# Performance work log

Measured on AMD Instinct MI355X. Metric: run time of the kernel, lower is better.

The kernel has to match this reference:

```python
import jax, jax.numpy as jnp
import numpy as np

VOCAB, EBD, ATT_H, R, T, IMG_C = 50257, 512, 512, 196, 1024, 512


def setup_inputs() -> dict:
    key = jax.random.key(0)
    ks = jax.random.split(key, 10)
    question = jax.random.randint(ks[0], (T,), 0, VOCAB)
    img_feat = jax.random.normal(ks[1], (R, IMG_C), dtype=jnp.float32)
    emb_table = (jax.random.normal(ks[2], (VOCAB, EBD), dtype=jnp.float32) * 0.02).at[0].set(0.0)  # padding_idx=0
    W_img = jax.random.normal(ks[3], (EBD, IMG_C), dtype=jnp.float32) * (1.0 / np.sqrt(IMG_C))
    b_img = jnp.zeros((EBD,), dtype=jnp.float32)
    W_ai = jax.random.normal(ks[4], (ATT_H, EBD), dtype=jnp.float32) * (1.0 / np.sqrt(EBD))  # att_img, no bias
    W_aw = jax.random.normal(ks[5], (ATT_H, EBD), dtype=jnp.float32) * (1.0 / np.sqrt(EBD))  # att_word
    b_aw = jnp.zeros((ATT_H,), dtype=jnp.float32)
    w_att = jax.random.normal(ks[6], (ATT_H,), dtype=jnp.float32) * (1.0 / np.sqrt(ATT_H))  # att -> scalar
    b_att = jnp.zeros((), dtype=jnp.float32)
    return {"question": question, "img_feat": img_feat, "emb_table": emb_table,
            "W_img": W_img, "b_img": b_img, "W_ai": W_ai, "W_aw": W_aw,
            "b_aw": b_aw, "w_att": w_att, "b_att": b_att}


def reference(question, img_feat, emb_table, W_img, b_img, W_ai, W_aw, b_aw, w_att, b_att):
    # img_feature = relu(Linear(512 -> ebd)(vgg_regions));  [R, EBD]
    img = jax.nn.relu(img_feat @ W_img.T + b_img)
    # per-word embeddings  [T, EBD]
    E = emb_table[question]
    # additive attention: tanh(attImg[r] + attWord[t]) . w_att + b_att  -> [T, R]
    AI = img @ W_ai.T                       # [R, H]
    AW = E @ W_aw.T + b_aw                  # [T, H]
    scores = jnp.einsum('trh,h->tr', jnp.tanh(AI[None, :, :] + AW[:, None, :]), w_att) + b_att
    w = jax.nn.softmax(scores, axis=-1)     # softmax over regions, [T, R]
    # weighted sum of img features, divided by n_regions (faithful to original)
    ctx = (w @ img) / img.shape[0]          # [T, EBD]
    # attedInput: concat(new_img_feature, word_emd)  [T, 2*EBD]
    return jnp.concatenate([ctx, E], axis=-1)
```

## Files before the change

### kernel.cpp

```cpp
#include <hip/hip_runtime.h>

#define PRESCALE 2.8853900817779268f

typedef short s16;
typedef unsigned short u16;
typedef unsigned int u32;
typedef __attribute__((ext_vector_type(8))) short short8v;
typedef __attribute__((ext_vector_type(4))) float f4;

#if __has_builtin(__builtin_amdgcn_exp2f)
#define EXP2(x) __builtin_amdgcn_exp2f(x)
#else
static __device__ inline float exp2_raw(float x){ float r; asm("v_exp_f32 %0, %1":"=v"(r):"v"(x)); return r; }
#define EXP2(x) exp2_raw(x)
#endif
#if __has_builtin(__builtin_amdgcn_rcpf)
#define RCP(x) __builtin_amdgcn_rcpf(x)
#else
static __device__ inline float rcp_raw(float x){ float r; asm("v_rcp_f32 %0, %1":"=v"(r):"v"(x)); return r; }
#define RCP(x) rcp_raw(x)
#endif

__device__ inline u32 cvt2(float lo, float hi){
  u32 r; asm("v_cvt_pk_bf16_f32 %0, %1, %2" : "=v"(r) : "v"(lo), "v"(hi)); return r;
}
__device__ inline f4 ldf4(const float* p){ return *reinterpret_cast<const f4*>(p); }
__device__ inline short8v cvt8(f4 a, f4 b){
  union { u32 u[4]; short8v s; } x;
  x.u[0] = cvt2(a.x, a.y); x.u[1] = cvt2(a.z, a.w);
  x.u[2] = cvt2(b.x, b.y); x.u[3] = cvt2(b.z, b.w);
  return x.s;
}

__global__ __launch_bounds__(256) void k_front2(
    const int* __restrict__ question, const float* __restrict__ img_feat,
    const float* __restrict__ emb,
    const float* __restrict__ W_img, const float* __restrict__ b_img,
    const float* __restrict__ W_aw,  const float* __restrict__ b_aw,
    float* __restrict__ img, float* __restrict__ AWT4, float* __restrict__ out){
  const int tid = threadIdx.x, w = tid>>6, l = tid&63;
  const int lr = l & 15, lg = l >> 4;

  if (blockIdx.x < 32){
    const int m0 = (blockIdx.x >> 3)*64 + (w>>1)*32;
    const int n0 = (blockIdx.x & 7)*64 + (w&1)*32;
    const float* pa0 = img_feat + (size_t)min(m0+lr,    195)*512 + lg*8;
    const float* pa1 = img_feat + (size_t)min(m0+16+lr, 195)*512 + lg*8;
    const float* pb0 = W_img + (size_t)(n0 + lr)*512 + lg*8;
    const float* pb1 = pb0 + (size_t)16*512;
    f4 acc[2][2] = {};
    for (int ks = 0; ks < 16; ++ks){
      const int o = ks*32;
      short8v a0 = cvt8(ldf4(pa0+o), ldf4(pa0+o+4));
      short8v a1 = cvt8(ldf4(pa1+o), ldf4(pa1+o+4));
      short8v b0 = cvt8(ldf4(pb0+o), ldf4(pb0+o+4));
      short8v b1 = cvt8(ldf4(pb1+o), ldf4(pb1+o+4));
      acc[0][0] = __builtin_amdgcn_mfma_f32_16x16x32_bf16(a0, b0, acc[0][0], 0, 0, 0);
      acc[0][1] = __builtin_amdgcn_mfma_f32_16x16x32_bf16(a0, b1, acc[0][1], 0, 0, 0);
      acc[1][0] = __builtin_amdgcn_mfma_f32_16x16x32_bf16(a1, b0, acc[1][0], 0, 0, 0);
      acc[1][1] = __builtin_amdgcn_mfma_f32_16x16x32_bf16(a1, b1, acc[1][1], 0, 0, 0);
    }
    #pragma unroll
    for (int i = 0; i < 2; ++i)
      #pragma unroll
      for (int j = 0; j < 2; ++j){
        const int nn = n0 + j*16 + lr;
        const float bc = b_img[nn];
        #pragma unroll
        for (int p = 0; p < 4; ++p){
          const int mm = m0 + i*16 + lg*4 + p;
          img[(size_t)mm*512 + nn] = fmaxf(acc[i][j][p] + bc, 0.f);
        }
      }
  } else if (blockIdx.x < 160){
    const int blk = blockIdx.x - 32;
    const int m0 = (blk >> 4)*64 + (w>>1)*32;
    const int n0 = (blk & 15)*64 + (w&1)*32;
    const int q0 = question[n0 + lr], q1 = question[n0 + 16 + lr];
    const float* pa0 = W_aw + (size_t)(m0 + lr)*512 + lg*8;
    const float* pa1 = pa0 + (size_t)16*512;
    const float* pe0 = emb + (size_t)q0*512 + lg*8;
    const float* pe1 = emb + (size_t)q1*512 + lg*8;
    f4 acc[2][2] = {};
    for (int ks = 0; ks < 16; ++ks){
      const int o = ks*32;
      short8v a0 = cvt8(ldf4(pa0+o), ldf4(pa0+o+4));
      short8v a1 = cvt8(ldf4(pa1+o), ldf4(pa1+o+4));
      short8v b0 = cvt8(ldf4(pe0+o), ldf4(pe0+o+4));
      short8v b1 = cvt8(ldf4(pe1+o), ldf4(pe1+o+4));
      acc[0][0] = __builtin_amdgcn_mfma_f32_16x16x32_bf16(a0, b0, acc[0][0], 0, 0, 0);
      acc[0][1] = __builtin_amdgcn_mfma_f32_16x16x32_bf16(a0, b1, acc[0][1], 0, 0, 0);
      acc[1][0] = __builtin_amdgcn_mfma_f32_16x16x32_bf16(a1, b0, acc[1][0], 0, 0, 0);
      acc[1][1] = __builtin_amdgcn_mfma_f32_16x16x32_bf16(a1, b1, acc[1][1], 0, 0, 0);
    }
    #pragma unroll
    for (int i = 0; i < 2; ++i){
      const int mb = m0 + i*16 + lg*4;
      #pragma unroll
      for (int j = 0; j < 2; ++j){
        const int nn = n0 + j*16 + lr;
        f4 o;
        #pragma unroll
        for (int p = 0; p < 4; ++p)
          o[p] = (acc[i][j][p] + b_aw[mb+p]) * PRESCALE;
        *reinterpret_cast<f4*>(AWT4 + (size_t)(mb>>2)*4096 + nn*4) = o;
      }
    }
  } else {
    const int t = (blockIdx.x - 160)*16 + (tid >> 4);
    const int c0 = (tid & 15)*32;
    const float* er = emb + (size_t)question[t]*512 + c0;
    float* orow = out + (size_t)t*1024 + 512 + c0;
    #pragma unroll
    for (int qd = 0; qd < 8; ++qd)
      *reinterpret_cast<f4*>(orow + qd*4) = ldf4(er + qd*4);
  }
}

__global__ __launch_bounds__(256) void k_ai(
    const float* __restrict__ img, const float* __restrict__ W_ai,
    float* __restrict__ AIp){
  const int tid = threadIdx.x, w = tid>>6, l = tid&63;
  const int lr = l & 15, lg = l >> 4;
  const int m0 = (blockIdx.x >> 3)*64 + (w>>1)*32;
  const int n0 = (blockIdx.x & 7)*64 + (w&1)*32;
  const int k0 = blockIdx.y*128;
  const float* pa0 = img  + (size_t)(m0 + lr)*512 + k0 + lg*8;
  const float* pa1 = pa0 + (size_t)16*512;
  const float* pb0 = W_ai + (size_t)(n0 + lr)*512 + k0 + lg*8;
  const float* pb1 = pb0 + (size_t)16*512;
  f4 acc[2][2] = {};
  #pragma unroll
  for (int ks = 0; ks < 4; ++ks){
    const int o = ks*32;
    short8v a0 = cvt8(ldf4(pa0+o), ldf4(pa0+o+4));
    short8v a1 = cvt8(ldf4(pa1+o), ldf4(pa1+o+4));
    short8v b0 = cvt8(ldf4(pb0+o), ldf4(pb0+o+4));
    short8v b1 = cvt8(ldf4(pb1+o), ldf4(pb1+o+4));
    acc[0][0] = __builtin_amdgcn_mfma_f32_16x16x32_bf16(a0, b0, acc[0][0], 0, 0, 0);
    acc[0][1] = __builtin_amdgcn_mfma_f32_16x16x32_bf16(a0, b1, acc[0][1], 0, 0, 0);
    acc[1][0] = __builtin_amdgcn_mfma_f32_16x16x32_bf16(a1, b0, acc[1][0], 0, 0, 0);
    acc[1][1] = __builtin_amdgcn_mfma_f32_16x16x32_bf16(a1, b1, acc[1][1], 0, 0, 0);
  }
  #pragma unroll
  for (int i = 0; i < 2; ++i)
    #pragma unroll
    for (int j = 0; j < 2; ++j){
      const int nn = n0 + j*16 + lr;
      #pragma unroll
      for (int p = 0; p < 4; ++p){
        const int mm = m0 + i*16 + lg*4 + p;
        AIp[((size_t)blockIdx.y<<17) + (size_t)mm*512 + nn] = acc[i][j][p] * PRESCALE;
      }
    }
}

#define RB5 5
__global__ __launch_bounds__(512) void k_score(
    const float* __restrict__ AIp, const float* __restrict__ AWT4,
    const float* __restrict__ w_att, float* __restrict__ STp){
  __shared__ float ais[RB5][64];
  __shared__ float wsh[64];
  const int tid = threadIdx.x, w = tid>>6, l = tid&63;
  const int rr = blockIdx.x, hc = blockIdx.y, th = blockIdx.z;
  const int r0 = rr*RB5, h0 = hc*64;
  if (tid < 80){
    const int i = tid >> 4, j = tid & 15;
    const int r = min(r0 + i, 195);
    f4 s = ldf4(AIp + (size_t)r*512 + h0 + j*4);
    #pragma unroll
    for (int kc = 1; kc < 4; ++kc)
      s += ldf4(AIp + ((size_t)kc<<17) + (size_t)r*512 + h0 + j*4);
    *reinterpret_cast<f4*>(&ais[i][j*4]) = s;
  } else if (tid < 96){
    const int j = tid - 80;
    *reinterpret_cast<f4*>(&wsh[j*4]) =
        *reinterpret_cast<const f4*>(w_att + h0 + j*4);
  }
  const int t = th*512 + w*64 + l;
  const int hg0 = hc*16;
  f4 awr[16];
  #pragma unroll
  for (int j = 0; j < 16; ++j)
    awr[j] = *reinterpret_cast<const f4*>(AWT4 + (size_t)(hg0+j)*4096 + t*4);
  __syncthreads();
  #pragma unroll
  for (int i = 0; i < RB5; ++i){
    const int r = r0 + i;
    if (r >= 196) break;
    float a0=0.f, a1=0.f, a2=0.f, a3=0.f;
    #pragma unroll
    for (int j = 0; j < 16; ++j){
      f4 av = *reinterpret_cast<const f4*>(&ais[i][j*4]);
      f4 wv = *reinterpret_cast<const f4*>(&wsh[j*4]);
      a0 += wv.x*RCP(EXP2(av.x+awr[j].x)+1.f);
      a1 += wv.y*RCP(EXP2(av.y+awr[j].y)+1.f);
      a2 += wv.z*RCP(EXP2(av.z+awr[j].z)+1.f);
      a3 += wv.w*RCP(EXP2(av.w+awr[j].w)+1.f);
    }
    STp[((size_t)hc<<18) + (size_t)r*1024 + t] = (a0+a1)+(a2+a3);
  }
}

__global__ __launch_bounds__(256) void k_ctx(
    const float* __restrict__ STp, const float* __restrict__ img,
    float* __restrict__ out){
  __shared__ float wgt[196][16];
  __shared__ float red[16][16];
  const int tid = threadIdx.x;
  const int t0 = blockIdx.x*16, e0 = blockIdx.y*64;
  const int rs = tid>>4, tl = tid&15;

  float sum = 0.f;
  for (int k = 0; k < 13; ++k){
    const int r = rs + 16*k;
    if (r < 196){
      float s = 0.f;
      #pragma unroll
      for (int c = 0; c < 8; ++c)
        s += STp[((size_t)c<<18) + (size_t)r*1024 + t0 + tl];
      float p = EXP2(-PRESCALE * s);
      wgt[r][tl] = p;
      sum += p;
    }
  }
  red[rs][tl] = sum;
  __syncthreads();
  if (tid < 16){
    float ss = 0.f;
    #pragma unroll
    for (int i = 0; i < 16; ++i) ss += red[i][tid];
    red[0][tid] = 1.f / (ss * 196.f);
  }
  __syncthreads();
  const float inv = red[0][tl];
  for (int k = 0; k < 13; ++k){
    const int r = rs + 16*k;
    if (r < 196) wgt[r][tl] *= inv;
  }
  __syncthreads();

  const int e = e0 + (tid & 63), tq = tid >> 6;
  float acc[4] = {0.f, 0.f, 0.f, 0.f};
  const float* ip = img + e;
  #pragma unroll 4
  for (int r = 0; r < 196; ++r){
    const float f = ip[(size_t)r*512];
    float4 w4 = *reinterpret_cast<const float4*>(&wgt[r][tq*4]);
    acc[0] += w4.x*f; acc[1] += w4.y*f; acc[2] += w4.z*f; acc[3] += w4.w*f;
  }
  #pragma unroll
  for (int j = 0; j < 4; ++j)
    out[(size_t)(t0 + tq*4 + j)*1024 + e] = acc[j];
}

extern "C" void kernel_launch(void* const* d_in, const int* in_sizes, int n_in,
                              void* d_out, int out_size, void* d_ws, size_t ws_size,
                              hipStream_t stream) {
  const int*   question = (const int*)d_in[0];
  const float* img_feat = (const float*)d_in[1];
  const float* emb      = (const float*)d_in[2];
  const float* W_img    = (const float*)d_in[3];
  const float* b_img    = (const float*)d_in[4];
  const float* W_ai     = (const float*)d_in[5];
  const float* W_aw     = (const float*)d_in[6];
  const float* b_aw     = (const float*)d_in[7];
  const float* w_att    = (const float*)d_in[8];
  float* out = (float*)d_out;

  char* ws = (char*)d_ws;
  float* img   = (float*)(ws);
  float* AIp   = (float*)(ws + 524288);
  float* AWT4  = (float*)(ws + 2621440);
  float* STp   = (float*)(ws + 4718592);

  hipLaunchKernelGGL(k_front2, dim3(224),    dim3(256), 0, stream,
                     question, img_feat, emb, W_img, b_img, W_aw, b_aw,
                     img, AWT4, out);
  hipLaunchKernelGGL(k_ai,     dim3(32,4),   dim3(256), 0, stream,
                     img, W_ai, AIp);
  hipLaunchKernelGGL(k_score,  dim3(40,8,2), dim3(512), 0, stream,
                     AIp, AWT4, w_att, STp);
  hipLaunchKernelGGL(k_ctx,    dim3(64,8),   dim3(256), 0, stream, STp, img, out);
}
```

Measured before the change: 76.34 us.

## Fuse AI projection into front kernel via split-K partials over LDS img tile

Removes the separate k_ai launch. Each image block now keeps its 64x64 relu(img) tile in LDS as bf16 and immediately multiplies it against the matching 64-column K-slice of W_ai. It writes 8 split-K partials of AI, which k_score now sums (8 partials instead of 4). This saves one kernel launch and the re-read of img from global memory. In exchange the 32 image blocks do much more work, k_score reads twice as many partials, and the workspace grows.

Result: slower. 86.27 us (+13.0%).

```diff
diff --git a/kernel.cpp b/kernel.cpp
--- a/kernel.cpp
+++ b/kernel.cpp
@@ -24,6 +24,11 @@
 __device__ inline u32 cvt2(float lo, float hi){
   u32 r; asm("v_cvt_pk_bf16_f32 %0, %1, %2" : "=v"(r) : "v"(lo), "v"(hi)); return r;
 }
+__device__ inline u16 f2bf(float f){
+  union{u32 i; float f;} v; v.f = f;
+  u32 r = v.i + 0x7fffu + ((v.i >> 16) & 1u);
+  return (u16)(r >> 16);
+}
 __device__ inline f4 ldf4(const float* p){ return *reinterpret_cast<const f4*>(p); }
 __device__ inline short8v cvt8(f4 a, f4 b){
   union { u32 u[4]; short8v s; } x;
@@ -32,46 +37,80 @@
   return x.s;
 }
 
-__global__ __launch_bounds__(256) void k_front2(
+#define LP 72
+
+__global__ __launch_bounds__(256) void k_front4(
     const int* __restrict__ question, const float* __restrict__ img_feat,
     const float* __restrict__ emb,
     const float* __restrict__ W_img, const float* __restrict__ b_img,
-    const float* __restrict__ W_aw,  const float* __restrict__ b_aw,
-    float* __restrict__ img, float* __restrict__ AWT4, float* __restrict__ out){
+    const float* __restrict__ W_ai,  const float* __restrict__ W_aw,
+    const float* __restrict__ b_aw,
+    float* __restrict__ img, float* __restrict__ AIp, float* __restrict__ AWT4,
+    float* __restrict__ out){
+  __shared__ u16 limg[64*LP];
   const int tid = threadIdx.x, w = tid>>6, l = tid&63;
   const int lr = l & 15, lg = l >> 4;
 
   if (blockIdx.x < 32){
-    const int m0 = (blockIdx.x >> 3)*64 + (w>>1)*32;
-    const int n0 = (blockIdx.x & 7)*64 + (w&1)*32;
-    const float* pa0 = img_feat + (size_t)min(m0+lr,    195)*512 + lg*8;
-    const float* pa1 = img_feat + (size_t)min(m0+16+lr, 195)*512 + lg*8;
-    const float* pb0 = W_img + (size_t)(n0 + lr)*512 + lg*8;
-    const float* pb1 = pb0 + (size_t)16*512;
-    f4 acc[2][2] = {};
-    for (int ks = 0; ks < 16; ++ks){
-      const int o = ks*32;
-      short8v a0 = cvt8(ldf4(pa0+o), ldf4(pa0+o+4));
-      short8v a1 = cvt8(ldf4(pa1+o), ldf4(pa1+o+4));
-      short8v b0 = cvt8(ldf4(pb0+o), ldf4(pb0+o+4));
-      short8v b1 = cvt8(ldf4(pb1+o), ldf4(pb1+o+4));
-      acc[0][0] = __builtin_amdgcn_mfma_f32_16x16x32_bf16(a0, b0, acc[0][0], 0, 0, 0);
-      acc[0][1] = __builtin_amdgcn_mfma_f32_16x16x32_bf16(a0, b1, acc[0][1], 0, 0, 0);
-      acc[1][0] = __builtin_amdgcn_mfma_f32_16x16x32_bf16(a1, b0, acc[1][0], 0, 0, 0);
-      acc[1][1] = __builtin_amdgcn_mfma_f32_16x16x32_bf16(a1, b1, acc[1][1], 0, 0, 0);
-    }
-    #pragma unroll
-    for (int i = 0; i < 2; ++i)
-      #pragma unroll
-      for (int j = 0; j < 2; ++j){
-        const int nn = n0 + j*16 + lr;
-        const float bc = b_img[nn];
-        #pragma unroll
-        for (int p = 0; p < 4; ++p){
-          const int mm = m0 + i*16 + lg*4 + p;
-          img[(size_t)mm*512 + nn] = fmaxf(acc[i][j][p] + bc, 0.f);
+    const int r0 = (blockIdx.x >> 3)*64;
+    const int eg = blockIdx.x & 7;
+    const int n0g = eg*64;
+    const int m0 = (w>>1)*32, n0 = (w&1)*32;
+    {
+      const float* pa0 = img_feat + (size_t)min(r0+m0+lr,    195)*512 + lg*8;
+      const float* pa1 = img_feat + (size_t)min(r0+m0+16+lr, 195)*512 + lg*8;
+      const float* pb0 = W_img + (size_t)(n0g + n0 + lr)*512 + lg*8;
+      const float* pb1 = pb0 + (size_t)16*512;
+      f4 acc[2][2] = {};
+      for (int ks = 0; ks < 16; ++ks){
+        const int o = ks*32;
+        short8v a0 = cvt8(ldf4(pa0+o), ldf4(pa0+o+4));
+        short8v a1 = cvt8(ldf4(pa1+o), ldf4(pa1+o+4));
+        short8v b0 = cvt8(ldf4(pb0+o), ldf4(pb0+o+4));
+        short8v b1 = cvt8(ldf4(pb1+o), ldf4(pb1+o+4));
+        acc[0][0] = __builtin_amdgcn_mfma_f32_16x16x32_bf16(a0, b0, acc[0][0], 0, 0, 0);
+        acc[0][1] = __builtin_amdgcn_mfma_f32_16x16x32_bf16(a0, b1, acc[0][1], 0, 0, 0);
+        acc[1][0] = __builtin_amdgcn_mfma_f32_16x16x32_bf16(a1, b0, acc[1][0], 0, 0, 0);
+        acc[1][1] = __builtin_amdgcn_mfma_f32_16x16x32_bf16(a1, b1, acc[1][1], 0, 0, 0);
+      }
+      #pragma unroll
+      for (int i = 0; i < 2; ++i)
+        #pragma unroll
+        for (int j = 0; j < 2; ++j){
+          const int el = n0 + j*16 + lr;
+          const float bc = b_img[n0g + el];
+          #pragma unroll
+          for (int p = 0; p < 4; ++p){
+            const int rl = m0 + i*16 + lg*4 + p;
+            float v = fmaxf(acc[i][j][p] + bc, 0.f);
+            img[(size_t)(r0+rl)*512 + n0g + el] = v;
+            limg[rl*LP + el] = f2bf(v);
+          }
+        }
+    }
+    __syncthreads();
+    const int h0w = w*128;
+    #pragma unroll
+    for (int rsub = 0; rsub < 4; ++rsub){
+      f4 acc2[8] = {};
+      #pragma unroll
+      for (int ks = 0; ks < 2; ++ks){
+        short8v a = *reinterpret_cast<const short8v*>(
+            &limg[(rsub*16 + lr)*LP + ks*32 + lg*8]);
+        #pragma unroll
+        for (int nf = 0; nf < 8; ++nf){
+          const float* pbn = W_ai + (size_t)(h0w + nf*16 + lr)*512 + n0g + ks*32 + lg*8;
+          short8v b = cvt8(ldf4(pbn), ldf4(pbn + 4));
+          acc2[nf] = __builtin_amdgcn_mfma_f32_16x16x32_bf16(a, b, acc2[nf], 0, 0, 0);
         }
       }
+      #pragma unroll
+      for (int nf = 0; nf < 8; ++nf)
+        #pragma unroll
+        for (int p = 0; p < 4; ++p)
+          AIp[((size_t)eg<<17) + (size_t)(r0 + rsub*16 + lg*4 + p)*512
+              + h0w + nf*16 + lr] = acc2[nf][p] * PRESCALE;
+    }
   } else if (blockIdx.x < 160){
     const int blk = blockIdx.x - 32;
     const int m0 = (blk >> 4)*64 + (w>>1)*32;
@@ -117,44 +156,6 @@
   }
 }
 
-__global__ __launch_bounds__(256) void k_ai(
-    const float* __restrict__ img, const float* __restrict__ W_ai,
-    float* __restrict__ AIp){
-  const int tid = threadIdx.x, w = tid>>6, l = tid&63;
-  const int lr = l & 15, lg = l >> 4;
-  const int m0 = (blockIdx.x >> 3)*64 + (w>>1)*32;
-  const int n0 = (blockIdx.x & 7)*64 + (w&1)*32;
-  const int k0 = blockIdx.y*128;
-  const float* pa0 = img  + (size_t)(m0 + lr)*512 + k0 + lg*8;
-  const float* pa1 = pa0 + (size_t)16*512;
-  const float* pb0 = W_ai + (size_t)(n0 + lr)*512 + k0 + lg*8;
-  const float* pb1 = pb0 + (size_t)16*512;
-  f4 acc[2][2] = {};
-  #pragma unroll
-  for (int ks = 0; ks < 4; ++ks){
-    const int o = ks*32;
-    short8v a0 = cvt8(ldf4(pa0+o), ldf4(pa0+o+4));
-    short8v a1 = cvt8(ldf4(pa1+o), ldf4(pa1+o+4));
-    short8v b0 = cvt8(ldf4(pb0+o), ldf4(pb0+o+4));
-    short8v b1 = cvt8(ldf4(pb1+o), ldf4(pb1+o+4));
-    acc[0][0] = __builtin_amdgcn_mfma_f32_16x16x32_bf16(a0, b0, acc[0][0], 0, 0, 0);
-    acc[0][1] = __builtin_amdgcn_mfma_f32_16x16x32_bf16(a0, b1, acc[0][1], 0, 0, 0);
-    acc[1][0] = __builtin_amdgcn_mfma_f32_16x16x32_bf16(a1, b0, acc[1][0], 0, 0, 0);
-    acc[1][1] = __builtin_amdgcn_mfma_f32_16x16x32_bf16(a1, b1, acc[1][1], 0, 0, 0);
-  }
-  #pragma unroll
-  for (int i = 0; i < 2; ++i)
-    #pragma unroll
-    for (int j = 0; j < 2; ++j){
-      const int nn = n0 + j*16 + lr;
-      #pragma unroll
-      for (int p = 0; p < 4; ++p){
-        const int mm = m0 + i*16 + lg*4 + p;
-        AIp[((size_t)blockIdx.y<<17) + (size_t)mm*512 + nn] = acc[i][j][p] * PRESCALE;
-      }
-    }
-}
-
 #define RB5 5
 __global__ __launch_bounds__(512) void k_score(
     const float* __restrict__ AIp, const float* __restrict__ AWT4,
@@ -169,7 +170,7 @@
     const int r = min(r0 + i, 195);
     f4 s = ldf4(AIp + (size_t)r*512 + h0 + j*4);
     #pragma unroll
-    for (int kc = 1; kc < 4; ++kc)
+    for (int kc = 1; kc < 8; ++kc)
       s += ldf4(AIp + ((size_t)kc<<17) + (size_t)r*512 + h0 + j*4);
     *reinterpret_cast<f4*>(&ais[i][j*4]) = s;
   } else if (tid < 96){
@@ -271,14 +272,12 @@
   char* ws = (char*)d_ws;
   float* img   = (float*)(ws);
   float* AIp   = (float*)(ws + 524288);
-  float* AWT4  = (float*)(ws + 2621440);
-  float* STp   = (float*)(ws + 4718592);
-
-  hipLaunchKernelGGL(k_front2, dim3(224),    dim3(256), 0, stream,
-                     question, img_feat, emb, W_img, b_img, W_aw, b_aw,
-                     img, AWT4, out);
-  hipLaunchKernelGGL(k_ai,     dim3(32,4),   dim3(256), 0, stream,
-                     img, W_ai, AIp);
+  float* AWT4  = (float*)(ws + 4718592);
+  float* STp   = (float*)(ws + 6815744);
+
+  hipLaunchKernelGGL(k_front4, dim3(224),    dim3(256), 0, stream,
+                     question, img_feat, emb, W_img, b_img, W_ai, W_aw, b_aw,
+                     img, AIp, AWT4, out);
   hipLaunchKernelGGL(k_score,  dim3(40,8,2), dim3(512), 0, stream,
                      AIp, AWT4, w_att, STp);
   hipLaunchKernelGGL(k_ctx,    dim3(64,8),   dim3(256), 0, stream, STp, img, out);
```
